# Kernel optimization log

Measured on AMD Instinct MI355X. Metric: run time of the kernel, lower is better.

## Reference

```python
import jax, jax.numpy as jnp
import numpy as np

N, E, D, H, O = 50000, 800000, 128, 256, 64
BN_EPS = 1e-5


def setup_inputs() -> dict:
    key = jax.random.key(0)
    ks = jax.random.split(key, 12)
    x_indices = jnp.arange(N, dtype=jnp.int64) if jax.config.jax_enable_x64 else jnp.arange(N, dtype=jnp.int32)
    ei = jax.random.randint(ks[0], (2, E), 0, N, dtype=jnp.int32)
    s = lambda k, shape, fan: jax.random.normal(k, shape, dtype=jnp.float32) * (1.0 / np.sqrt(fan))
    return {
        "x_indices": x_indices,
        "ei": ei,
        "emb": jax.random.normal(ks[1], (N, D), dtype=jnp.float32),
        "W1": s(ks[2], (D, H), D), "b1": jnp.zeros((H,), jnp.float32),
        "g1": jnp.ones((H,), jnp.float32), "be1": jnp.zeros((H,), jnp.float32),
        "W2": s(ks[3], (H, H), H), "b2": jnp.zeros((H,), jnp.float32),
        "g2": jnp.ones((H,), jnp.float32), "be2": jnp.zeros((H,), jnp.float32),
        "W3": s(ks[4], (H, O), H), "b3": jnp.zeros((O,), jnp.float32),
    }


def reference(x_indices, ei, emb, W1, b1, g1, be1, W2, b2, g2, be2, W3, b3):
    n = emb.shape[0]
    # GCN normalization with self-loops (PyG GCNConv default):
    loop = jnp.arange(n, dtype=ei.dtype)
    row = jnp.concatenate([ei[0], loop])  # source
    col = jnp.concatenate([ei[1], loop])  # target (aggregation index)
    deg = jax.ops.segment_sum(jnp.ones_like(col, dtype=emb.dtype), col, num_segments=n)
    dinv = jnp.where(deg > 0, 1.0 / jnp.sqrt(jnp.maximum(deg, 1.0)), 0.0)
    norm = dinv[row] * dinv[col]  # [E+N]

    def conv(x, W, b):
        xl = x @ W                                   # [N, d_out]
        msg = xl[row] * norm[:, None]                # gather + scale
        return jax.ops.segment_sum(msg, col, num_segments=n) + b  # scatter-add

    def bn(x, g, be):  # batch-stat BatchNorm1d (training-mode stats)
        m = jnp.mean(x, axis=0)
        v = jnp.var(x, axis=0)
        return (x - m) * (g / jnp.sqrt(v + BN_EPS)) + be

    x = emb[x_indices]
    x = jax.nn.relu(bn(conv(x, W1, b1), g1, be1))
    x = jax.nn.relu(bn(conv(x, W2, b2), g2, be2))
    return conv(x, W3, b3)
```

## Files before the change

kernel.cpp:

```cpp
#include <hip/hip_runtime.h>
#include <hip/hip_bf16.h>

#define Dk 128
#define Hk 256
#define Ok 64
#define BN_EPS 1e-5f

typedef __attribute__((ext_vector_type(8))) short short8;
typedef __attribute__((ext_vector_type(4))) float f32x4;

static __device__ __forceinline__ float bf2f(ushort u) {
    union { uint32_t i; float f; } c; c.i = ((uint32_t)u) << 16; return c.f;
}
static __device__ __forceinline__ ushort f2bf(float f) {
    union { float f; uint32_t u; } c; c.f = f;
    return (ushort)((c.u + 0x7fffu + ((c.u >> 16) & 1u)) >> 16);
}


__global__ void count_kernel(const int* __restrict__ col, int* __restrict__ cnt, int E) {
    int e = blockIdx.x * blockDim.x + threadIdx.x;
    if (e < E) atomicAdd(&cnt[col[e]], 1);
}

__global__ void dinv_bsum_kernel(const int* __restrict__ cnt, float* __restrict__ dinv,
                                 int* __restrict__ fillc, int* __restrict__ bsum, int n) {
    __shared__ int sm[256];
    int i = blockIdx.x * 256 + threadIdx.x;
    int c = (i < n) ? cnt[i] : 0;
    if (i < n) { dinv[i] = rsqrtf((float)c + 1.0f); fillc[i] = 0; }
    sm[threadIdx.x] = c;
    __syncthreads();
    for (int s = 128; s; s >>= 1) {
        if (threadIdx.x < s) sm[threadIdx.x] += sm[threadIdx.x + s];
        __syncthreads();
    }
    if (!threadIdx.x) bsum[blockIdx.x] = sm[0];
}

__global__ void scan_base_kernel(int* __restrict__ bsum, int nb) {
    __shared__ int sm[256];
    int t = threadIdx.x;
    int carry = 0;
    for (int base = 0; base < nb; base += 256) {
        int i = base + t;
        int v = (i < nb) ? bsum[i] : 0;
        sm[t] = v;
        __syncthreads();
        for (int s = 1; s < 256; s <<= 1) {
            int add = (t >= s) ? sm[t - s] : 0;
            __syncthreads();
            sm[t] += add;
            __syncthreads();
        }
        if (i < nb) bsum[i] = carry + sm[t] - v;
        int tot = sm[255];
        __syncthreads();
        carry += tot;
    }
}

__global__ void scan_final_kernel(const int* __restrict__ cnt, const int* __restrict__ bbase,
                                  int* __restrict__ offv, int n) {
    __shared__ int sm[256];
    int t = threadIdx.x, i = blockIdx.x * 256 + t;
    int v = (i < n) ? cnt[i] : 0;
    sm[t] = v;
    __syncthreads();
    for (int s = 1; s < 256; s <<= 1) {
        int add = (t >= s) ? sm[t - s] : 0;
        __syncthreads();
        sm[t] += add;
        __syncthreads();
    }
    if (i < n) offv[i + 1] = bbase[blockIdx.x] + sm[t];
    if (i == 0) offv[0] = 0;
}

__global__ void fill_kernel(const int* __restrict__ row, const int* __restrict__ col,
                            const int* __restrict__ off, int* __restrict__ fillc,
                            const float* __restrict__ dinv, int2* __restrict__ ep, int E) {
    int e = blockIdx.x * blockDim.x + threadIdx.x;
    if (e < E) {
        int c = col[e], r = row[e];
        int p = atomicAdd(&fillc[c], 1);
        ep[off[c] + p] = make_int2(r, __float_as_int(dinv[r]));
    }
}


#define W1SZ (Dk * Hk)
#define W2SZ (Hk * Hk)
#define W3SZ (Hk * Ok)
#define WBLK ((W1SZ + W2SZ + W3SZ) / 256)
#define STATSP_FLOATS (2 * 64 * 512)

__global__ void cvt_all_kernel(const float* __restrict__ emb, const int* __restrict__ xidx,
                               ushort* __restrict__ embb,
                               const float* __restrict__ W1, const float* __restrict__ W2,
                               const float* __restrict__ W3, ushort* __restrict__ W1t,
                               ushort* __restrict__ W2t, ushort* __restrict__ W3t,
                               float* __restrict__ statsP, int n) {
    const int embBlocks = (n * (Dk / 8) + 255) >> 8;
    int bid = blockIdx.x;
    if (bid < embBlocks) {
        int gid = bid * 256 + threadIdx.x;
        int total = n * (Dk / 8);
        if (gid >= total) return;
        int node = gid >> 4, seg = gid & 15;
        int src = xidx[node];
        const float* p = &emb[(size_t)src * Dk + seg * 8];
        float4 lo = *(const float4*)p, hi = *(const float4*)(p + 4);
        ushort r[8] = {f2bf(lo.x), f2bf(lo.y), f2bf(lo.z), f2bf(lo.w),
                       f2bf(hi.x), f2bf(hi.y), f2bf(hi.z), f2bf(hi.w)};
        *(short8*)&embb[(size_t)gid * 8] = *(short8*)r;
        return;
    }
    bid -= embBlocks;
    if (bid < WBLK) {
        int gid = bid * 256 + threadIdx.x;
        if (gid < W1SZ) {
            int c = gid / Dk, k = gid - c * Dk;
            W1t[gid] = f2bf(W1[(size_t)k * Hk + c]);
        } else if (gid < W1SZ + W2SZ) {
            int idx = gid - W1SZ;
            int c = idx / Hk, k = idx - c * Hk;
            W2t[idx] = f2bf(W2[(size_t)k * Hk + c]);
        } else {
            int idx = gid - W1SZ - W2SZ;
            int c = idx / Hk, k = idx - c * Hk;
            W3t[idx] = f2bf(W3[(size_t)k * Ok + c]);
        }
        return;
    }
    bid -= WBLK;
    int idx = bid * 1024 + threadIdx.x * 4;
    if (idx < STATSP_FLOATS)
        *(float4*)&statsP[idx] = make_float4(0.f, 0.f, 0.f, 0.f);
}

__global__ void bn_finalize_kernel(const float* __restrict__ statsP, const float* __restrict__ g,
                                   const float* __restrict__ be, float* __restrict__ ss,
                                   float invn) {
    int f = threadIdx.x;
    float sum = 0.f, sq = 0.f;
    for (int s = 0; s < 64; ++s) {
        sum += statsP[s * 512 + f];
        sq  += statsP[s * 512 + 256 + f];
    }
    float mean = sum * invn;
    float var = sq * invn - mean * mean;
    float sc = g[f] * rsqrtf(var + BN_EPS);
    ss[f] = sc;
    ss[256 + f] = fmaf(-mean, sc, be[f]);
}


template<int KD, int BNT, bool STATS, bool BIAS, bool BN_A>
__global__ __launch_bounds__(256) void gemm128(
    const ushort* __restrict__ A, const ushort* __restrict__ Wt,
    ushort* __restrict__ Cout, int n, int Hout,
    const float* __restrict__ bias, float* __restrict__ statsP,
    const float* __restrict__ ss)
{
    constexpr int WN = (BNT == 128) ? 2 : 1;
    constexpr int MR = (BNT == 128) ? 4 : 2;
    constexpr int NR = 4;
    constexpr int TILE = (128 + BNT) * 32;
    constexpr int NT = KD / 32;
    __shared__ ushort lds[2 * TILE];
    __shared__ float ssc[BN_A ? KD : 1];
    __shared__ float ssh[BN_A ? KD : 1];

    const int tid = threadIdx.x;
    const int lane = tid & 63, wid = tid >> 6;
    const int wr = wid / WN, wc = wid % WN;
    const int lr = lane & 15, lg = lane >> 4;
    const int bm = blockIdx.x * 128;
    const int bn = blockIdx.y * BNT;

    if (BN_A) {
        for (int f = tid; f < KD; f += 256) {
            ssc[f] = ss[f];
            ssh[f] = ss[KD + f];
        }
        __syncthreads();
    }

    auto stage = [&](int buf, int k0) {
        ushort* As = lds + buf * TILE;
        ushort* Bs = As + 128 * 32;
        #pragma unroll
        for (int c = 0; c < 2; ++c) {
            int boff = wid * 2048 + c * 1024 + lane * 16;
            int row = boff >> 6;
            int k8 = (boff >> 4) & 3;
            int grow = bm + row; if (grow >= n) grow = n - 1;
            const ushort* src = &A[(size_t)grow * KD + k0 + k8 * 8];
            if (BN_A) {
                short8 av = *(const short8*)src;
                ushort r[8];
                #pragma unroll
                for (int j = 0; j < 8; ++j) {
                    int kf = k0 + k8 * 8 + j;
                    float v = bf2f((ushort)av[j]);
                    r[j] = f2bf(fmaxf(fmaf(v, ssc[kf], ssh[kf]), 0.f));
                }
                *(short8*)&As[row * 32 + k8 * 8] = *(short8*)r;
            } else {
                __builtin_amdgcn_global_load_lds(
                    (const __attribute__((address_space(1))) void*)src,
                    (__attribute__((address_space(3))) void*)&As[(wid * 2048 + c * 1024) >> 1],
                    16, 0, 0);
            }
        }
        constexpr int BC = BNT * 64 / 4096;
        #pragma unroll
        for (int c = 0; c < BC; ++c) {
            int boff = wid * (BNT * 16) + c * 1024 + lane * 16;
            int col = boff >> 6;
            int k8 = (boff >> 4) & 3;
            const ushort* src = &Wt[(size_t)(bn + col) * KD + k0 + k8 * 8];
            __builtin_amdgcn_global_load_lds(
                (const __attribute__((address_space(1))) void*)src,
                (__attribute__((address_space(3))) void*)&Bs[(wid * (BNT * 16) + c * 1024) >> 1],
                16, 0, 0);
        }
    };

    f32x4 acc[MR][NR] = {};

    stage(0, 0);
    __syncthreads();
    int cur = 0;
    for (int t = 0; t < NT; ++t) {
        if (t + 1 < NT) stage(cur ^ 1, (t + 1) * 32);
        ushort* As = lds + cur * TILE;
        ushort* Bs = As + 128 * 32;
        short8 af[MR], bfr[NR];
        #pragma unroll
        for (int m = 0; m < MR; ++m)
            af[m] = *(const short8*)&As[(wr * MR * 16 + m * 16 + lr) * 32 + lg * 8];
        #pragma unroll
        for (int nn = 0; nn < NR; ++nn)
            bfr[nn] = *(const short8*)&Bs[(wc * NR * 16 + nn * 16 + lr) * 32 + lg * 8];
        #pragma unroll
        for (int m = 0; m < MR; ++m)
            #pragma unroll
            for (int nn = 0; nn < NR; ++nn)
                acc[m][nn] = __builtin_amdgcn_mfma_f32_16x16x32_bf16(af[m], bfr[nn], acc[m][nn], 0, 0, 0);
        __syncthreads();
        cur ^= 1;
    }

    float s[NR], q[NR];
    #pragma unroll
    for (int nn = 0; nn < NR; ++nn) { s[nn] = 0.f; q[nn] = 0.f; }
    #pragma unroll
    for (int nn = 0; nn < NR; ++nn) {
        int col = bn + wc * NR * 16 + nn * 16 + lr;
        float bv = BIAS ? bias[col] : 0.f;
        #pragma unroll
        for (int m = 0; m < MR; ++m) {
            #pragma unroll
            for (int i = 0; i < 4; ++i) {
                int row = bm + wr * MR * 16 + m * 16 + lg * 4 + i;
                if (row < n) {
                    float v = acc[m][nn][i] + bv;
                    Cout[(size_t)row * Hout + col] = f2bf(v);
                    if (STATS) { s[nn] += v; q[nn] += v * v; }
                }
            }
        }
    }
    if (STATS) {
        float* sp = statsP + (size_t)(blockIdx.x & 63) * 512;
        #pragma unroll
        for (int nn = 0; nn < NR; ++nn) {
            s[nn] += __shfl_xor(s[nn], 16);
            q[nn] += __shfl_xor(q[nn], 16);
            s[nn] += __shfl_xor(s[nn], 32);
            q[nn] += __shfl_xor(q[nn], 32);
            if (lg == 0) {
                int col = bn + wc * NR * 16 + nn * 16 + lr;
                atomicAdd(&sp[col], s[nn]);
                atomicAdd(&sp[256 + col], q[nn]);
            }
        }
    }
}


template<int FH, int LPN, int MODE>
__global__ __launch_bounds__(256) void agg_kernel(
    const ushort* __restrict__ x, const int2* __restrict__ ep, const int* __restrict__ off,
    const float* __restrict__ dinv, const float* __restrict__ ss,
    const float* __restrict__ bias, void* __restrict__ outp, int n)
{
    constexpr int VEC = FH / LPN;
    constexpr int NPW = 64 / LPN;
    constexpr int NPB = 4 * NPW;
    const int tid = threadIdx.x;
    const int lane = tid & 63;
    const int wid = tid >> 6;
    const int sub = lane / LPN;
    const int flane = lane % LPN;
    const int node = blockIdx.x * NPB + wid * NPW + sub;
    if (node >= n) return;
    const int fb = flane * VEC;
    const ushort* __restrict__ xb = x + fb;

    float sc[VEC], sh[VEC];
    if (MODE == 1) {
        float4 c4 = *(const float4*)&ss[fb];
        float4 h4 = *(const float4*)&ss[FH + fb];
        sc[0] = c4.x; sc[1] = c4.y; sc[2] = c4.z; sc[3] = c4.w;
        sh[0] = h4.x; sh[1] = h4.y; sh[2] = h4.z; sh[3] = h4.w;
    }
    auto xform = [&](ushort u, int v) -> float {
        float val = bf2f(u);
        if (MODE == 1) val = fmaxf(fmaf(val, sc[v], sh[v]), 0.f);
        return val;
    };

    float di = dinv[node];
    float acc[VEC];
    {
        ushort4 t = *(const ushort4*)&xb[(size_t)node * FH];
        acc[0] = di * xform(t.x, 0); acc[1] = di * xform(t.y, 1);
        acc[2] = di * xform(t.z, 2); acc[3] = di * xform(t.w, 3);
    }
    const int e1 = off[node + 1];
    int e = off[node];
    for (; e + 8 <= e1; e += 8) {
        int2 p[8];
        ushort4 t[8];
        #pragma unroll
        for (int j = 0; j < 8; ++j) p[j] = ep[e + j];
        #pragma unroll
        for (int j = 0; j < 8; ++j) t[j] = *(const ushort4*)&xb[(size_t)p[j].x * FH];
        #pragma unroll
        for (int j = 0; j < 8; ++j) {
            float w = __int_as_float(p[j].y);
            acc[0] = fmaf(w, xform(t[j].x, 0), acc[0]);
            acc[1] = fmaf(w, xform(t[j].y, 1), acc[1]);
            acc[2] = fmaf(w, xform(t[j].z, 2), acc[2]);
            acc[3] = fmaf(w, xform(t[j].w, 3), acc[3]);
        }
    }
    for (; e + 2 <= e1; e += 2) {
        int2 p0 = ep[e], p1 = ep[e + 1];
        ushort4 t0 = *(const ushort4*)&xb[(size_t)p0.x * FH];
        ushort4 t1 = *(const ushort4*)&xb[(size_t)p1.x * FH];
        float w0 = __int_as_float(p0.y), w1 = __int_as_float(p1.y);
        acc[0] = fmaf(w0, xform(t0.x, 0), acc[0]); acc[1] = fmaf(w0, xform(t0.y, 1), acc[1]);
        acc[2] = fmaf(w0, xform(t0.z, 2), acc[2]); acc[3] = fmaf(w0, xform(t0.w, 3), acc[3]);
        acc[0] = fmaf(w1, xform(t1.x, 0), acc[0]); acc[1] = fmaf(w1, xform(t1.y, 1), acc[1]);
        acc[2] = fmaf(w1, xform(t1.z, 2), acc[2]); acc[3] = fmaf(w1, xform(t1.w, 3), acc[3]);
    }
    if (e < e1) {
        int2 pp = ep[e];
        ushort4 tt = *(const ushort4*)&xb[(size_t)pp.x * FH];
        float w = __int_as_float(pp.y);
        acc[0] = fmaf(w, xform(tt.x, 0), acc[0]); acc[1] = fmaf(w, xform(tt.y, 1), acc[1]);
        acc[2] = fmaf(w, xform(tt.z, 2), acc[2]); acc[3] = fmaf(w, xform(tt.w, 3), acc[3]);
    }
    if (MODE == 2) {
        float4 bv = *(const float4*)&bias[fb];
        float4 res;
        res.x = fmaf(di, acc[0], bv.x); res.y = fmaf(di, acc[1], bv.y);
        res.z = fmaf(di, acc[2], bv.z); res.w = fmaf(di, acc[3], bv.w);
        *(float4*)((float*)outp + (size_t)node * FH + fb) = res;
    } else {
        ushort4 o;
        o.x = f2bf(di * acc[0]); o.y = f2bf(di * acc[1]);
        o.z = f2bf(di * acc[2]); o.w = f2bf(di * acc[3]);
        *(ushort4*)((ushort*)outp + (size_t)node * FH + fb) = o;
    }
}


extern "C" void kernel_launch(void* const* d_in, const int* in_sizes, int n_in,
                              void* d_out, int out_size, void* d_ws, size_t ws_size,
                              hipStream_t stream) {
    const int*   x_idx = (const int*)d_in[0];
    const int*   ei    = (const int*)d_in[1];
    const float* emb   = (const float*)d_in[2];
    const float* W1    = (const float*)d_in[3];
    const float* b1    = (const float*)d_in[4];
    const float* g1    = (const float*)d_in[5];
    const float* be1   = (const float*)d_in[6];
    const float* W2    = (const float*)d_in[7];
    const float* b2    = (const float*)d_in[8];
    const float* g2    = (const float*)d_in[9];
    const float* be2   = (const float*)d_in[10];
    const float* W3    = (const float*)d_in[11];
    const float* b3    = (const float*)d_in[12];

    const int N = in_sizes[0];
    const int E = in_sizes[1] / 2;
    const int* erow = ei;
    const int* ecol = ei + E;

    char* p = (char*)d_ws;
    auto alloc = [&](size_t bytes) { char* q = p; p += (bytes + 255) & ~(size_t)255; return q; };
    const int nb = (N + 255) / 256;
    float*  dinv  = (float*) alloc((size_t)N * 4);
    int*    cnt   = (int*)   alloc((size_t)N * 4);
    int*    off   = (int*)   alloc((size_t)(N + 1) * 4);
    int*    fillc = (int*)   alloc((size_t)N * 4);
    int*    bsum  = (int*)   alloc((size_t)nb * 4);
    int2*   ep    = (int2*)  alloc((size_t)E * 8);
    float*  statsP= (float*) alloc((size_t)STATSP_FLOATS * 4);
    float*  stats1P = statsP, *stats2P = statsP + 64 * 512;
    float*  ss1   = (float*) alloc(512 * 4);
    float*  ss2   = (float*) alloc(512 * 4);
    ushort* W1t   = (ushort*)alloc((size_t)Dk * Hk * 2);
    ushort* W2t   = (ushort*)alloc((size_t)Hk * Hk * 2);
    ushort* W3t   = (ushort*)alloc((size_t)Hk * Ok * 2);
    ushort* bufU  = (ushort*)alloc((size_t)N * Hk * 2);
    ushort* embb  = bufU;
    ushort* agg1b = bufU + (size_t)N * Dk;
    ushort* conv2b= bufU;
    ushort* conv1b= (ushort*)alloc((size_t)N * Hk * 2);
    ushort* agg2b = (ushort*)alloc((size_t)N * Hk * 2);
    ushort* xl3b  = (ushort*)alloc((size_t)N * Ok * 2);

    const float invn = 1.0f / (float)N;

    hipMemsetAsync(cnt, 0, (size_t)N * 4, stream);
    count_kernel<<<(E + 255) / 256, 256, 0, stream>>>(ecol, cnt, E);
    dinv_bsum_kernel<<<nb, 256, 0, stream>>>(cnt, dinv, fillc, bsum, N);
    scan_base_kernel<<<1, 256, 0, stream>>>(bsum, nb);
    scan_final_kernel<<<nb, 256, 0, stream>>>(cnt, bsum, off, N);
    fill_kernel<<<(E + 255) / 256, 256, 0, stream>>>(erow, ecol, off, fillc, dinv, ep, E);

    const int embBlocks = (N * (Dk / 8) + 255) / 256;
    cvt_all_kernel<<<embBlocks + WBLK + (STATSP_FLOATS + 1023) / 1024, 256, 0, stream>>>(
        emb, x_idx, embb, W1, W2, W3, W1t, W2t, W3t, statsP, N);

    const int rb128 = (N + 127) / 128;

    agg_kernel<Dk, 32, 0><<<(N + 7) / 8, 256, 0, stream>>>(
        embb, ep, off, dinv, nullptr, nullptr, agg1b, N);
    gemm128<Dk, 128, true, true, false><<<dim3(rb128, Hk / 128), 256, 0, stream>>>(
        agg1b, W1t, conv1b, N, Hk, b1, stats1P, nullptr);
    bn_finalize_kernel<<<1, 256, 0, stream>>>(stats1P, g1, be1, ss1, invn);

    agg_kernel<Hk, 64, 1><<<(N + 3) / 4, 256, 0, stream>>>(
        conv1b, ep, off, dinv, ss1, nullptr, agg2b, N);
    gemm128<Hk, 128, true, true, false><<<dim3(rb128, Hk / 128), 256, 0, stream>>>(
        agg2b, W2t, conv2b, N, Hk, b2, stats2P, nullptr);
    bn_finalize_kernel<<<1, 256, 0, stream>>>(stats2P, g2, be2, ss2, invn);

    gemm128<Hk, 64, false, false, true><<<dim3(rb128, 1), 256, 0, stream>>>(
        conv2b, W3t, xl3b, N, Ok, nullptr, nullptr, ss2);
    agg_kernel<Ok, 16, 2><<<(N + 15) / 16, 256, 0, stream>>>(
        xl3b, ep, off, dinv, nullptr, b3, d_out, N);
}
```

Before: 287.5 us.

## Fuse BN finalize into consumers, merge count and convert, restructure aggregation

Folds the edge-count pass into the conversion kernel and replaces the single-block base scan with a per-block prefix computed inside the final scan kernel. BN statistics now use 8 slices instead of 64 partial slots, and the finalize step is recomputed per block inside the consumers, which drops two tiny launches. The aggregation kernel now gives one wave per node and splits edges across lane groups with shuffle reductions, in place of packing several nodes per wave. The trade-off is more atomic contention on fewer stats slots and repeated finalize work in every block.

```diff
diff --git a/kernel.cpp b/kernel.cpp
--- a/kernel.cpp
+++ b/kernel.cpp
@@ -5,6 +5,7 @@
 #define Hk 256
 #define Ok 64
 #define BN_EPS 1e-5f
+#define NSLICE 8
 
 typedef __attribute__((ext_vector_type(8))) short short8;
 typedef __attribute__((ext_vector_type(4))) float f32x4;
@@ -15,77 +16,6 @@
 static __device__ __forceinline__ ushort f2bf(float f) {
     union { float f; uint32_t u; } c; c.f = f;
     return (ushort)((c.u + 0x7fffu + ((c.u >> 16) & 1u)) >> 16);
-}
-
-
-__global__ void count_kernel(const int* __restrict__ col, int* __restrict__ cnt, int E) {
-    int e = blockIdx.x * blockDim.x + threadIdx.x;
-    if (e < E) atomicAdd(&cnt[col[e]], 1);
-}
-
-__global__ void dinv_bsum_kernel(const int* __restrict__ cnt, float* __restrict__ dinv,
-                                 int* __restrict__ fillc, int* __restrict__ bsum, int n) {
-    __shared__ int sm[256];
-    int i = blockIdx.x * 256 + threadIdx.x;
-    int c = (i < n) ? cnt[i] : 0;
-    if (i < n) { dinv[i] = rsqrtf((float)c + 1.0f); fillc[i] = 0; }
-    sm[threadIdx.x] = c;
-    __syncthreads();
-    for (int s = 128; s; s >>= 1) {
-        if (threadIdx.x < s) sm[threadIdx.x] += sm[threadIdx.x + s];
-        __syncthreads();
-    }
-    if (!threadIdx.x) bsum[blockIdx.x] = sm[0];
-}
-
-__global__ void scan_base_kernel(int* __restrict__ bsum, int nb) {
-    __shared__ int sm[256];
-    int t = threadIdx.x;
-    int carry = 0;
-    for (int base = 0; base < nb; base += 256) {
-        int i = base + t;
-        int v = (i < nb) ? bsum[i] : 0;
-        sm[t] = v;
-        __syncthreads();
-        for (int s = 1; s < 256; s <<= 1) {
-            int add = (t >= s) ? sm[t - s] : 0;
-            __syncthreads();
-            sm[t] += add;
-            __syncthreads();
-        }
-        if (i < nb) bsum[i] = carry + sm[t] - v;
-        int tot = sm[255];
-        __syncthreads();
-        carry += tot;
-    }
-}
-
-__global__ void scan_final_kernel(const int* __restrict__ cnt, const int* __restrict__ bbase,
-                                  int* __restrict__ offv, int n) {
-    __shared__ int sm[256];
-    int t = threadIdx.x, i = blockIdx.x * 256 + t;
-    int v = (i < n) ? cnt[i] : 0;
-    sm[t] = v;
-    __syncthreads();
-    for (int s = 1; s < 256; s <<= 1) {
-        int add = (t >= s) ? sm[t - s] : 0;
-        __syncthreads();
-        sm[t] += add;
-        __syncthreads();
-    }
-    if (i < n) offv[i + 1] = bbase[blockIdx.x] + sm[t];
-    if (i == 0) offv[0] = 0;
-}
-
-__global__ void fill_kernel(const int* __restrict__ row, const int* __restrict__ col,
-                            const int* __restrict__ off, int* __restrict__ fillc,
-                            const float* __restrict__ dinv, int2* __restrict__ ep, int E) {
-    int e = blockIdx.x * blockDim.x + threadIdx.x;
-    if (e < E) {
-        int c = col[e], r = row[e];
-        int p = atomicAdd(&fillc[c], 1);
-        ep[off[c] + p] = make_int2(r, __float_as_int(dinv[r]));
-    }
 }
 
 
@@ -93,16 +23,24 @@
 #define W2SZ (Hk * Hk)
 #define W3SZ (Hk * Ok)
 #define WBLK ((W1SZ + W2SZ + W3SZ) / 256)
-#define STATSP_FLOATS (2 * 64 * 512)
-
-__global__ void cvt_all_kernel(const float* __restrict__ emb, const int* __restrict__ xidx,
-                               ushort* __restrict__ embb,
-                               const float* __restrict__ W1, const float* __restrict__ W2,
-                               const float* __restrict__ W3, ushort* __restrict__ W1t,
-                               ushort* __restrict__ W2t, ushort* __restrict__ W3t,
-                               float* __restrict__ statsP, int n) {
+#define STATSP_FLOATS (2 * NSLICE * 512)
+
+__global__ void count_cvt_kernel(const int* __restrict__ ecol, int* __restrict__ cnt, int E,
+                                 const float* __restrict__ emb, const int* __restrict__ xidx,
+                                 ushort* __restrict__ embb,
+                                 const float* __restrict__ W1, const float* __restrict__ W2,
+                                 const float* __restrict__ W3, ushort* __restrict__ W1t,
+                                 ushort* __restrict__ W2t, ushort* __restrict__ W3t,
+                                 float* __restrict__ statsP, int n) {
+    const int cntBlocks = (E + 255) >> 8;
     const int embBlocks = (n * (Dk / 8) + 255) >> 8;
     int bid = blockIdx.x;
+    if (bid < cntBlocks) {
+        int e = bid * 256 + threadIdx.x;
+        if (e < E) atomicAdd(&cnt[ecol[e]], 1);
+        return;
+    }
+    bid -= cntBlocks;
     if (bid < embBlocks) {
         int gid = bid * 256 + threadIdx.x;
         int total = n * (Dk / 8);
@@ -139,20 +77,61 @@
         *(float4*)&statsP[idx] = make_float4(0.f, 0.f, 0.f, 0.f);
 }
 
-__global__ void bn_finalize_kernel(const float* __restrict__ statsP, const float* __restrict__ g,
-                                   const float* __restrict__ be, float* __restrict__ ss,
-                                   float invn) {
-    int f = threadIdx.x;
-    float sum = 0.f, sq = 0.f;
-    for (int s = 0; s < 64; ++s) {
-        sum += statsP[s * 512 + f];
-        sq  += statsP[s * 512 + 256 + f];
-    }
-    float mean = sum * invn;
-    float var = sq * invn - mean * mean;
-    float sc = g[f] * rsqrtf(var + BN_EPS);
-    ss[f] = sc;
-    ss[256 + f] = fmaf(-mean, sc, be[f]);
+__global__ void dinv_bsum_kernel(const int* __restrict__ cnt, float* __restrict__ dinv,
+                                 int* __restrict__ fillc, int* __restrict__ bsum, int n) {
+    __shared__ int sm[256];
+    int i = blockIdx.x * 256 + threadIdx.x;
+    int c = (i < n) ? cnt[i] : 0;
+    if (i < n) { dinv[i] = rsqrtf((float)c + 1.0f); fillc[i] = 0; }
+    sm[threadIdx.x] = c;
+    __syncthreads();
+    for (int s = 128; s; s >>= 1) {
+        if (threadIdx.x < s) sm[threadIdx.x] += sm[threadIdx.x + s];
+        __syncthreads();
+    }
+    if (!threadIdx.x) bsum[blockIdx.x] = sm[0];
+}
+
+__global__ void scan_off_kernel(const int* __restrict__ cnt, const int* __restrict__ bsum,
+                                int* __restrict__ offv, int n) {
+    __shared__ int sm[256];
+    __shared__ int sbase;
+    int t = threadIdx.x, bidx = blockIdx.x;
+    int part = 0;
+    for (int j = t; j < bidx; j += 256) part += bsum[j];
+    sm[t] = part;
+    __syncthreads();
+    for (int s = 128; s; s >>= 1) {
+        if (t < s) sm[t] += sm[t + s];
+        __syncthreads();
+    }
+    if (t == 0) sbase = sm[0];
+    __syncthreads();
+    int base = sbase;
+    __syncthreads();
+    int i = bidx * 256 + t;
+    int v = (i < n) ? cnt[i] : 0;
+    sm[t] = v;
+    __syncthreads();
+    for (int s = 1; s < 256; s <<= 1) {
+        int add = (t >= s) ? sm[t - s] : 0;
+        __syncthreads();
+        sm[t] += add;
+        __syncthreads();
+    }
+    if (i < n) offv[i + 1] = base + sm[t];
+    if (i == 0) offv[0] = 0;
+}
+
+__global__ void fill_kernel(const int* __restrict__ row, const int* __restrict__ col,
+                            const int* __restrict__ off, int* __restrict__ fillc,
+                            const float* __restrict__ dinv, int2* __restrict__ ep, int E) {
+    int e = blockIdx.x * blockDim.x + threadIdx.x;
+    if (e < E) {
+        int c = col[e], r = row[e];
+        int p = atomicAdd(&fillc[c], 1);
+        ep[off[c] + p] = make_int2(r, __float_as_int(dinv[r]));
+    }
 }
 
 
@@ -161,7 +140,8 @@
     const ushort* __restrict__ A, const ushort* __restrict__ Wt,
     ushort* __restrict__ Cout, int n, int Hout,
     const float* __restrict__ bias, float* __restrict__ statsP,
-    const float* __restrict__ ss)
+    const float* __restrict__ statsInP, const float* __restrict__ g,
+    const float* __restrict__ be, float invn)
 {
     constexpr int WN = (BNT == 128) ? 2 : 1;
     constexpr int MR = (BNT == 128) ? 4 : 2;
@@ -181,8 +161,17 @@
 
     if (BN_A) {
         for (int f = tid; f < KD; f += 256) {
-            ssc[f] = ss[f];
-            ssh[f] = ss[KD + f];
+            float sum = 0.f, sq = 0.f;
+            #pragma unroll
+            for (int s = 0; s < NSLICE; ++s) {
+                sum += statsInP[s * 2 * KD + f];
+                sq  += statsInP[s * 2 * KD + KD + f];
+            }
+            float mean = sum * invn;
+            float var = sq * invn - mean * mean;
+            float sc = g[f] * rsqrtf(var + BN_EPS);
+            ssc[f] = sc;
+            ssh[f] = fmaf(-mean, sc, be[f]);
         }
         __syncthreads();
     }
@@ -274,7 +263,7 @@
         }
     }
     if (STATS) {
-        float* sp = statsP + (size_t)(blockIdx.x & 63) * 512;
+        float* sp = statsP + (size_t)(blockIdx.x & (NSLICE - 1)) * 2 * 256;
         #pragma unroll
         for (int nn = 0; nn < NR; ++nn) {
             s[nn] += __shfl_xor(s[nn], 16);
@@ -291,31 +280,49 @@
 }
 
 
-template<int FH, int LPN, int MODE>
+template<int FH, int EPI, int MODE>
 __global__ __launch_bounds__(256) void agg_kernel(
     const ushort* __restrict__ x, const int2* __restrict__ ep, const int* __restrict__ off,
-    const float* __restrict__ dinv, const float* __restrict__ ss,
+    const float* __restrict__ dinv, const float* __restrict__ statsP,
+    const float* __restrict__ g, const float* __restrict__ be, float invn,
     const float* __restrict__ bias, void* __restrict__ outp, int n)
 {
-    constexpr int VEC = FH / LPN;
-    constexpr int NPW = 64 / LPN;
-    constexpr int NPB = 4 * NPW;
+    constexpr int LPG = 64 / EPI;
+    constexpr int VEC = FH / LPG;
+    constexpr int U = 8 / EPI;
+    __shared__ float sbn[(MODE == 1) ? 2 * FH : 1];
     const int tid = threadIdx.x;
+
+    if (MODE == 1) {
+        for (int f = tid; f < FH; f += 256) {
+            float sum = 0.f, sq = 0.f;
+            #pragma unroll
+            for (int s = 0; s < NSLICE; ++s) {
+                sum += statsP[s * 2 * FH + f];
+                sq  += statsP[s * 2 * FH + FH + f];
+            }
+            float mean = sum * invn;
+            float var = sq * invn - mean * mean;
+            float sc = g[f] * rsqrtf(var + BN_EPS);
+            sbn[f] = sc;
+            sbn[FH + f] = fmaf(-mean, sc, be[f]);
+        }
+        __syncthreads();
+    }
+
     const int lane = tid & 63;
     const int wid = tid >> 6;
-    const int sub = lane / LPN;
-    const int flane = lane % LPN;
-    const int node = blockIdx.x * NPB + wid * NPW + sub;
+    const int node = blockIdx.x * 4 + wid;
     if (node >= n) return;
+    const int grp = lane / LPG;
+    const int flane = lane % LPG;
     const int fb = flane * VEC;
     const ushort* __restrict__ xb = x + fb;
 
     float sc[VEC], sh[VEC];
     if (MODE == 1) {
-        float4 c4 = *(const float4*)&ss[fb];
-        float4 h4 = *(const float4*)&ss[FH + fb];
-        sc[0] = c4.x; sc[1] = c4.y; sc[2] = c4.z; sc[3] = c4.w;
-        sh[0] = h4.x; sh[1] = h4.y; sh[2] = h4.z; sh[3] = h4.w;
+        #pragma unroll
+        for (int v = 0; v < VEC; ++v) { sc[v] = sbn[fb + v]; sh[v] = sbn[FH + fb + v]; }
     }
     auto xform = [&](ushort u, int v) -> float {
         float val = bf2f(u);
@@ -324,58 +331,65 @@
     };
 
     float di = dinv[node];
-    float acc[VEC];
-    {
+    float acc[VEC] = {0.f, 0.f, 0.f, 0.f};
+    if (EPI == 1 || grp == 0) {
         ushort4 t = *(const ushort4*)&xb[(size_t)node * FH];
         acc[0] = di * xform(t.x, 0); acc[1] = di * xform(t.y, 1);
         acc[2] = di * xform(t.z, 2); acc[3] = di * xform(t.w, 3);
     }
     const int e1 = off[node + 1];
-    int e = off[node];
-    for (; e + 8 <= e1; e += 8) {
-        int2 p[8];
-        ushort4 t[8];
-        #pragma unroll
-        for (int j = 0; j < 8; ++j) p[j] = ep[e + j];
-        #pragma unroll
-        for (int j = 0; j < 8; ++j) t[j] = *(const ushort4*)&xb[(size_t)p[j].x * FH];
-        #pragma unroll
-        for (int j = 0; j < 8; ++j) {
-            float w = __int_as_float(p[j].y);
-            acc[0] = fmaf(w, xform(t[j].x, 0), acc[0]);
-            acc[1] = fmaf(w, xform(t[j].y, 1), acc[1]);
-            acc[2] = fmaf(w, xform(t[j].z, 2), acc[2]);
-            acc[3] = fmaf(w, xform(t[j].w, 3), acc[3]);
-        }
-    }
-    for (; e + 2 <= e1; e += 2) {
-        int2 p0 = ep[e], p1 = ep[e + 1];
-        ushort4 t0 = *(const ushort4*)&xb[(size_t)p0.x * FH];
-        ushort4 t1 = *(const ushort4*)&xb[(size_t)p1.x * FH];
-        float w0 = __int_as_float(p0.y), w1 = __int_as_float(p1.y);
-        acc[0] = fmaf(w0, xform(t0.x, 0), acc[0]); acc[1] = fmaf(w0, xform(t0.y, 1), acc[1]);
-        acc[2] = fmaf(w0, xform(t0.z, 2), acc[2]); acc[3] = fmaf(w0, xform(t0.w, 3), acc[3]);
-        acc[0] = fmaf(w1, xform(t1.x, 0), acc[0]); acc[1] = fmaf(w1, xform(t1.y, 1), acc[1]);
-        acc[2] = fmaf(w1, xform(t1.z, 2), acc[2]); acc[3] = fmaf(w1, xform(t1.w, 3), acc[3]);
-    }
-    if (e < e1) {
-        int2 pp = ep[e];
-        ushort4 tt = *(const ushort4*)&xb[(size_t)pp.x * FH];
-        float w = __int_as_float(pp.y);
-        acc[0] = fmaf(w, xform(tt.x, 0), acc[0]); acc[1] = fmaf(w, xform(tt.y, 1), acc[1]);
-        acc[2] = fmaf(w, xform(tt.z, 2), acc[2]); acc[3] = fmaf(w, xform(tt.w, 3), acc[3]);
-    }
-    if (MODE == 2) {
-        float4 bv = *(const float4*)&bias[fb];
-        float4 res;
-        res.x = fmaf(di, acc[0], bv.x); res.y = fmaf(di, acc[1], bv.y);
-        res.z = fmaf(di, acc[2], bv.z); res.w = fmaf(di, acc[3], bv.w);
-        *(float4*)((float*)outp + (size_t)node * FH + fb) = res;
-    } else {
-        ushort4 o;
-        o.x = f2bf(di * acc[0]); o.y = f2bf(di * acc[1]);
-        o.z = f2bf(di * acc[2]); o.w = f2bf(di * acc[3]);
-        *(ushort4*)((ushort*)outp + (size_t)node * FH + fb) = o;
+    int b = off[node];
+    for (; b + 8 <= e1; b += 8) {
+        int2 p[U];
+        ushort4 t[U];
+        #pragma unroll
+        for (int u = 0; u < U; ++u) p[u] = ep[b + grp + u * EPI];
+        #pragma unroll
+        for (int u = 0; u < U; ++u) t[u] = *(const ushort4*)&xb[(size_t)p[u].x * FH];
+        #pragma unroll
+        for (int u = 0; u < U; ++u) {
+            float w = __int_as_float(p[u].y);
+            acc[0] = fmaf(w, xform(t[u].x, 0), acc[0]);
+            acc[1] = fmaf(w, xform(t[u].y, 1), acc[1]);
+            acc[2] = fmaf(w, xform(t[u].z, 2), acc[2]);
+            acc[3] = fmaf(w, xform(t[u].w, 3), acc[3]);
+        }
+    }
+    if (b < e1) {
+        #pragma unroll
+        for (int u = 0; u < U; ++u) {
+            int idx = b + grp + u * EPI;
+            bool ok = idx < e1;
+            int2 pp = ep[ok ? idx : b];
+            ushort4 tt = *(const ushort4*)&xb[(size_t)pp.x * FH];
+            float w = ok ? __int_as_float(pp.y) : 0.f;
+            acc[0] = fmaf(w, xform(tt.x, 0), acc[0]);
+            acc[1] = fmaf(w, xform(tt.y, 1), acc[1]);
+            acc[2] = fmaf(w, xform(tt.z, 2), acc[2]);
+            acc[3] = fmaf(w, xform(tt.w, 3), acc[3]);
+        }
+    }
+    if (EPI == 4) {
+        #pragma unroll
+        for (int v = 0; v < VEC; ++v) acc[v] += __shfl_xor(acc[v], 16);
+    }
+    if (EPI >= 2) {
+        #pragma unroll
+        for (int v = 0; v < VEC; ++v) acc[v] += __shfl_xor(acc[v], 32);
+    }
+    if (grp == 0) {
+        if (MODE == 2) {
+            float4 bv = *(const float4*)&bias[fb];
+            float4 res;
+            res.x = fmaf(di, acc[0], bv.x); res.y = fmaf(di, acc[1], bv.y);
+            res.z = fmaf(di, acc[2], bv.z); res.w = fmaf(di, acc[3], bv.w);
+            *(float4*)((float*)outp + (size_t)node * FH + fb) = res;
+        } else {
+            ushort4 o;
+            o.x = f2bf(di * acc[0]); o.y = f2bf(di * acc[1]);
+            o.z = f2bf(di * acc[2]); o.w = f2bf(di * acc[3]);
+            *(ushort4*)((ushort*)outp + (size_t)node * FH + fb) = o;
+        }
     }
 }
 
@@ -412,9 +426,7 @@
     int*    bsum  = (int*)   alloc((size_t)nb * 4);
     int2*   ep    = (int2*)  alloc((size_t)E * 8);
     float*  statsP= (float*) alloc((size_t)STATSP_FLOATS * 4);
-    float*  stats1P = statsP, *stats2P = statsP + 64 * 512;
-    float*  ss1   = (float*) alloc(512 * 4);
-    float*  ss2   = (float*) alloc(512 * 4);
+    float*  stats1P = statsP, *stats2P = statsP + NSLICE * 512;
     ushort* W1t   = (ushort*)alloc((size_t)Dk * Hk * 2);
     ushort* W2t   = (ushort*)alloc((size_t)Hk * Hk * 2);
     ushort* W3t   = (ushort*)alloc((size_t)Hk * Ok * 2);
@@ -429,32 +441,30 @@
     const float invn = 1.0f / (float)N;
 
     hipMemsetAsync(cnt, 0, (size_t)N * 4, stream);
-    count_kernel<<<(E + 255) / 256, 256, 0, stream>>>(ecol, cnt, E);
+    const int cntBlocks = (E + 255) / 256;
+    const int embBlocks = (N * (Dk / 8) + 255) / 256;
+    count_cvt_kernel<<<cntBlocks + embBlocks + WBLK + (STATSP_FLOATS + 1023) / 1024,
+                       256, 0, stream>>>(
+        ecol, cnt, E, emb, x_idx, embb, W1, W2, W3, W1t, W2t, W3t, statsP, N);
     dinv_bsum_kernel<<<nb, 256, 0, stream>>>(cnt, dinv, fillc, bsum, N);
-    scan_base_kernel<<<1, 256, 0, stream>>>(bsum, nb);
-    scan_final_kernel<<<nb, 256, 0, stream>>>(cnt, bsum, off, N);
+    scan_off_kernel<<<nb, 256, 0, stream>>>(cnt, bsum, off, N);
     fill_kernel<<<(E + 255) / 256, 256, 0, stream>>>(erow, ecol, off, fillc, dinv, ep, E);
 
-    const int embBlocks = (N * (Dk / 8) + 255) / 256;
-    cvt_all_kernel<<<embBlocks + WBLK + (STATSP_FLOATS + 1023) / 1024, 256, 0, stream>>>(
-        emb, x_idx, embb, W1, W2, W3, W1t, W2t, W3t, statsP, N);
-
     const int rb128 = (N + 127) / 128;
-
-    agg_kernel<Dk, 32, 0><<<(N + 7) / 8, 256, 0, stream>>>(
-        embb, ep, off, dinv, nullptr, nullptr, agg1b, N);
+    const int aggBlocks = (N + 3) / 4;
+
+    agg_kernel<Dk, 2, 0><<<aggBlocks, 256, 0, stream>>>(
+        embb, ep, off, dinv, nullptr, nullptr, nullptr, 0.f, nullptr, agg1b, N);
     gemm128<Dk, 128, true, true, false><<<dim3(rb128, Hk / 128), 256, 0, stream>>>(
-        agg1b, W1t, conv1b, N, Hk, b1, stats1P, nullptr);
-    bn_finalize_kernel<<<1, 256, 0, stream>>>(stats1P, g1, be1, ss1, invn);
-
-    agg_kernel<Hk, 64, 1><<<(N + 3) / 4, 256, 0, stream>>>(
-        conv1b, ep, off, dinv, ss1, nullptr, agg2b, N);
+        agg1b, W1t, conv1b, N, Hk, b1, stats1P, nullptr, nullptr, nullptr, 0.f);
+
+    agg_kernel<Hk, 1, 1><<<aggBlocks, 256, 0, stream>>>(
+        conv1b, ep, off, dinv, stats1P, g1, be1, invn, nullptr, agg2b, N);
     gemm128<Hk, 128, true, true, false><<<dim3(rb128, Hk / 128), 256, 0, stream>>>(
-        agg2b, W2t, conv2b, N, Hk, b2, stats2P, nullptr);
-    bn_finalize_kernel<<<1, 256, 0, stream>>>(stats2P, g2, be2, ss2, invn);
+        agg2b, W2t, conv2b, N, Hk, b2, stats2P, nullptr, nullptr, nullptr, 0.f);
 
     gemm128<Hk, 64, false, false, true><<<dim3(rb128, 1), 256, 0, stream>>>(
-        conv2b, W3t, xl3b, N, Ok, nullptr, nullptr, ss2);
-    agg_kernel<Ok, 16, 2><<<(N + 15) / 16, 256, 0, stream>>>(
-        xl3b, ep, off, dinv, nullptr, b3, d_out, N);
-}
+        conv2b, W3t, xl3b, N, Ok, nullptr, nullptr, stats2P, g2, be2, invn);
+    agg_kernel<Ok, 4, 2><<<aggBlocks, 256, 0, stream>>>(
+        xl3b, ep, off, dinv, nullptr, nullptr, nullptr, 0.f, b3, d_out, N);
+}
```

Measured after the change: 296.0 us. 3.0% more time.
